# Kernel optimization log

Hardware: AMD Instinct MI355X
Metric: run time of the kernel (lower is better)

Reference implementation:

```python
import jax, jax.numpy as jnp
import numpy as np

N = 4096; IN = 78; OUT = 11
HN = 256; HB = 128; HM = 64; HV = 256; HU = 128
NOTES_PER_BEAT = 8; BEATS_PER_MEASURE = 4
NB = N // NOTES_PER_BEAT; NM = NB // BEATS_PER_MEASURE
UIN = 2*HN + 2*HB + 2*HM + 2*HV + OUT + 2 + 1 + 2   # output-LSTM input = 1424
BT_IN = 2*HB + 1 + 1 + 2 + 3 + (OUT - 1)            # tempo-LSTM input = 273
QPM_PRIMO_IDX = 5; TEMPO_IDX = 28


def _u(key, shape, k):
    return jax.random.uniform(key, shape, minval=-k, maxval=k, dtype=jnp.float32)


def _lstm_p(key, din, h, bidir):
    k = 1.0 / np.sqrt(h); n = 2 if bidir else 1
    k1, k2, k3 = jax.random.split(key, 3)
    Wi = _u(k1, (n, 4*h, din), k); Wh = _u(k2, (n, 4*h, h), k); b = _u(k3, (n, 4*h), k)
    if not bidir:
        Wi, Wh, b = Wi[0], Wh[0], b[0]
    return Wi, Wh, b


def _lin_p(key, din, dout):
    k = 1.0 / np.sqrt(din)
    k1, k2 = jax.random.split(key)
    return _u(k1, (dout, din), k), _u(k2, (dout,), k)


def setup_inputs():
    ks = jax.random.split(jax.random.key(0), 20)
    inp = {}
    inp['x'] = jax.random.normal(ks[0], (1, N, IN), dtype=jnp.float32)
    inp['y'] = jax.random.normal(ks[1], (1, 1, OUT), dtype=jnp.float32)
    inp['beat_ids'] = (jnp.arange(N) // NOTES_PER_BEAT).astype(jnp.int32)
    inp['measure_ids'] = (jnp.arange(N) // (NOTES_PER_BEAT * BEATS_PER_MEASURE)).astype(jnp.int32)
    inp['note_Wi'], inp['note_Wh'], inp['note_b'] = _lstm_p(ks[2], IN, HN, True)
    inp['voice_Wi'], inp['voice_Wh'], inp['voice_b'] = _lstm_p(ks[3], IN, HV, True)
    inp['beat_Wi'], inp['beat_Wh'], inp['beat_b'] = _lstm_p(ks[4], 2*HN, HB, True)
    inp['meas_Wi'], inp['meas_Wh'], inp['meas_b'] = _lstm_p(ks[5], 2*HB, HM, True)
    inp['Wba'], inp['bba'] = _lin_p(ks[6], 2*HN, 2*HN)
    inp['Wma'], inp['bma'] = _lin_p(ks[7], 2*HB, 2*HB)
    inp['Wta'], inp['bta'] = _lin_p(ks[8], OUT-1, OUT-1)
    inp['out_Wi'], inp['out_Wh'], inp['out_b'] = _lstm_p(ks[9], UIN, HU, False)
    inp['Wfc'], inp['bfc'] = _lin_p(ks[10], HU + UIN, OUT-1)
    inp['bt_Wi'], inp['bt_Wh'], inp['bt_b'] = _lstm_p(ks[11], BT_IN, HB, False)
    inp['Wt1'], inp['bt1'] = _lin_p(ks[12], HB, HB)
    inp['Wt2'], inp['bt2'] = _lin_p(ks[13], HB, 1)
    return inp


def _cell(h, c, xt, Wi, Wh, b):
    g = Wi @ xt + Wh @ h + b
    i, f, gg, o = jnp.split(g, 4)
    c2 = jax.nn.sigmoid(f) * c + jax.nn.sigmoid(i) * jnp.tanh(gg)
    return jax.nn.sigmoid(o) * jnp.tanh(c2), c2


def _lstm(xs, Wi, Wh, b, reverse=False):
    H = Wh.shape[-1]
    def step(carry, xt):
        h, c = _cell(carry[0], carry[1], xt, Wi, Wh, b)
        return (h, c), h
    init = (jnp.zeros(H, xs.dtype), jnp.zeros(H, xs.dtype))
    _, hs = jax.lax.scan(step, init, xs, reverse=reverse)
    return hs


def _bilstm(xs, Wi, Wh, b):
    return jnp.concatenate([_lstm(xs, Wi[0], Wh[0], b[0]),
                            _lstm(xs, Wi[1], Wh[1], b[1], reverse=True)], axis=-1)


def _seg_attn(h, seg, nseg, W, b):
    # sum_with_attention: softmax over group members, per feature dim (torch softmax dim=0)
    logits = h @ W.T + b
    m = jax.ops.segment_max(logits, seg, num_segments=nseg)
    e = jnp.exp(logits - m[seg])
    s = jax.ops.segment_sum(e, seg, num_segments=nseg)
    return jax.ops.segment_sum(h * (e / s[seg]), seg, num_segments=nseg)


def _forward(x, y, beat_ids, measure_ids, note_Wi, note_Wh, note_b, voice_Wi, voice_Wh, voice_b,
             beat_Wi, beat_Wh, beat_b, meas_Wi, meas_Wh, meas_b, Wba, bba, Wma, bma, Wta, bta,
             out_Wi, out_Wh, out_b, Wfc, bfc, bt_Wi, bt_Wh, bt_b, Wt1, bt1, Wt2, bt2):
    xs = x[0]                                   # [N, IN]
    note_h = _bilstm(xs, note_Wi, note_Wh, note_b)          # [N, 2*HN]
    voice_h = _bilstm(xs, voice_Wi, voice_Wh, voice_b)      # single voice -> whole seq
    beat_nodes = _seg_attn(note_h, beat_ids, NB, Wba, bba)  # [NB, 2*HN]
    beat_h = _bilstm(beat_nodes, beat_Wi, beat_Wh, beat_b)  # [NB, 2*HB]
    meas_of_beat = jax.ops.segment_min(measure_ids, beat_ids, num_segments=NB)
    meas_nodes = _seg_attn(beat_h, meas_of_beat, NM, Wma, bma)
    meas_h = _bilstm(meas_nodes, meas_Wi, meas_Wh, meas_b)  # [NM, 2*HM]

    qpm_primo = x[:, 0, QPM_PRIMO_IDX]          # (1,)
    tempo_primo = x[0, 0, -2:]                  # (2,)
    btv = xs[:, TEMPO_IDX:TEMPO_IDX+3]          # [N, 3]
    beat_pn = beat_h[beat_ids]                  # [N, 2*HB]
    meas_pn = meas_h[measure_ids]               # [N, 2*HM]
    is_b = jnp.concatenate([jnp.array([True]), beat_ids[1:] > beat_ids[:-1]])
    y_tail = y[0, 0, 1:]

    def step(carry, inp):
        buf, count, pt, th, tc, oh, oc, po, pv = carry
        nh_i, bh_i, mh_i, vh_i, btv_i, isb = inp
        # --- beat boundary: tempo attention + tempo LSTM step ---
        mask = jnp.arange(NOTES_PER_BEAT) < count
        logits = jnp.where(mask[:, None], buf @ Wta.T + bta, -1e9)
        att = jax.nn.softmax(logits, axis=0)
        result_node = jnp.where(count > 0, jnp.sum(buf * att, axis=0), y_tail)
        cat = jnp.concatenate([bh_i, pt, qpm_primo, tempo_primo, btv_i, result_node])
        nth, ntc = _cell(th, tc, cat, bt_Wi, bt_Wh, bt_b)
        tmp = Wt2 @ jax.nn.relu(Wt1 @ nth + bt1) + bt2     # (1,)
        th = jnp.where(isb, nth, th); tc = jnp.where(isb, ntc, tc)
        pt = jnp.where(isb, tmp, pt)
        buf = jnp.where(isb, jnp.zeros_like(buf), buf)
        count = jnp.where(isb, 0, count)
        comb = jnp.concatenate([nh_i, bh_i, mh_i, vh_i, po, pv, qpm_primo, tempo_primo])  # (UIN,)
        noh, noc = _cell(oh, oc, comb, out_Wi, out_Wh, out_b)
        out_fc = Wfc @ jnp.concatenate([noh, comb]) + bfc   # (OUT-1,)
        out = jnp.concatenate([pt, out_fc])                 # (OUT,)
        buf = buf.at[count].set(out_fc)
        return (buf, count + 1, pt, th, tc, noh, noc, out, out_fc[:2]), out

    carry0 = (jnp.zeros((NOTES_PER_BEAT, OUT-1)), jnp.array(0, jnp.int32), y[:, 0, 0],
              jnp.zeros(HB), jnp.zeros(HB), jnp.zeros(HU), jnp.zeros(HU), y[0, 0, :], jnp.zeros(2))
    _, outs = jax.lax.scan(step, carry0, (note_h, beat_pn, meas_pn, voice_h, btv, is_b))
    return outs[None], note_h[None]


def reference(x, y, beat_ids, measure_ids, note_Wi, note_Wh, note_b, voice_Wi, voice_Wh, voice_b,
              beat_Wi, beat_Wh, beat_b, meas_Wi, meas_Wh, meas_b, Wba, bba, Wma, bma, Wta, bta,
              out_Wi, out_Wh, out_b, Wfc, bfc, bt_Wi, bt_Wh, bt_b, Wt1, bt1, Wt2, bt2):
    return _forward(x, y, beat_ids, measure_ids, note_Wi, note_Wh, note_b, voice_Wi, voice_Wh, voice_b,
                    beat_Wi, beat_Wh, beat_b, meas_Wi, meas_Wh, meas_b, Wba, bba, Wma, bma, Wta, bta,
                    out_Wi, out_Wh, out_b, Wfc, bfc, bt_Wi, bt_Wh, bt_b, Wt1, bt1, Wt2, bt2)
```

## Files before the change

kernel.cpp:

```cpp
#include <hip/hip_runtime.h>
#include <hip/hip_bf16.h>

typedef unsigned int u32;
typedef _Float16 h16;
typedef __attribute__((ext_vector_type(2))) _Float16 h16x2;

union U4 { uint4 u; h16x2 p[4]; };

static __device__ __forceinline__ float sigm(float x){ return 1.0f / (1.0f + __expf(-x)); }
static __device__ __forceinline__ float ftanh(float x){ return 1.0f - 2.0f/(1.0f + __expf(2.0f*x)); }
static __device__ __forceinline__ h16x2 f2h2(float a, float b){
  h16x2 r; r[0] = (h16)a; r[1] = (h16)b; return r;
}
static __device__ __forceinline__ void pinv(h16x2 &x){
  u32 t = __builtin_bit_cast(u32, x);
  asm volatile("" : "+v"(t));
  x = __builtin_bit_cast(h16x2, t);
}

#if defined(__has_builtin)
#if __has_builtin(__builtin_amdgcn_fdot2)
#define FDOT2_NATIVE 1
#endif
#endif
static __device__ __forceinline__ float fdot2(h16x2 a, h16x2 b, float c){
#ifdef FDOT2_NATIVE
  return __builtin_amdgcn_fdot2(a, b, c, false);
#else
  return c + (float)a[0]*(float)b[0] + (float)a[1]*(float)b[1];
#endif
}

#define NT 4096
#define OUTS_OFF 45056

__global__ __launch_bounds__(256) void k0_prep(
    const float* __restrict__ noteWh, const float* __restrict__ voiceWh,
    const float* __restrict__ outWi,  const float* __restrict__ Wfc,
    h16* __restrict__ WhF, h16* __restrict__ outWiF, h16* __restrict__ WfcKF)
{
  const int NWH = 4*1024*256;
  const int NOW = 512*1416;
  const int NFC = 10*1416;
  for (int i = blockIdx.x*256 + threadIdx.x; i < NWH + NOW + NFC; i += gridDim.x*256) {
    if (i < NWH) {
      int dir = i >> 18;
      int rem = i & 262143;
      const float* src = (dir < 2) ? noteWh : voiceWh;
      WhF[i] = (h16)src[((dir & 1) << 18) + rem];
    } else if (i < NWH + NOW) {
      int j = i - NWH;
      int r = j / 1416, c = j - r*1416;
      float v = 0.f;
      if (c < 1408) v = outWi[(size_t)r*1424 + c];
      else if (c < 1411) v = outWi[(size_t)r*1424 + 1421 + (c-1408)];
      outWiF[j] = (h16)v;
    } else {
      int j = i - NWH - NOW;
      int r = j / 1416, c = j - r*1416;
      float v = 0.f;
      if (c < 1408) v = Wfc[(size_t)r*1552 + 128 + c];
      else if (c < 1411) v = Wfc[(size_t)r*1552 + 1549 + (c-1408)];
      WfcKF[j] = (h16)v;
    }
  }
}

__global__ __launch_bounds__(256) void k1_xgates(
    const float* __restrict__ x,
    const float* __restrict__ noteWi, const float* __restrict__ noteB,
    const float* __restrict__ voiceWi, const float* __restrict__ voiceB,
    h16* __restrict__ preNV)
{
  const int dir = blockIdx.y;
  const int t0  = blockIdx.x * 16;
  const int tid = threadIdx.x;
  __shared__ float xs[16][80];
  for (int i = tid; i < 16*78; i += 256) {
    int tt = i / 78, j = i - tt*78;
    xs[tt][j] = x[(size_t)(t0+tt)*78 + j];
  }
  __syncthreads();
  const float* Wi = (dir < 2) ? noteWi : voiceWi;
  const float* B  = (dir < 2) ? noteB  : voiceB;
  const int dw = dir & 1;
  for (int gc = 0; gc < 4; ++gc) {
    int g = gc*256 + tid;
    const float* row = Wi + ((size_t)dw*1024 + g)*78;
    float bias = B[dw*1024 + g];
    float acc[16];
#pragma unroll
    for (int tt=0; tt<16; ++tt) acc[tt] = bias;
#pragma unroll 6
    for (int j=0; j<78; ++j) {
      float w = row[j];
#pragma unroll
      for (int tt=0; tt<16; ++tt)
        acc[tt] += w*xs[tt][j];
    }
#pragma unroll
    for (int tt=0; tt<16; ++tt)
      preNV[((size_t)dir*NT + (t0+tt))*1024 + g] = (h16)acc[tt];
  }
}

__global__ __launch_bounds__(512) void k2_nvrec(
    const h16* __restrict__ WhF,
    const h16* __restrict__ preNV,
    float* __restrict__ note_h,
    float* __restrict__ voice_h,
    float* __restrict__ out_noteh)
{
  const int dir = blockIdx.x;
  const int L = threadIdx.x;
  const int r0 = L, r1 = L + 512;
  const h16* Wb = WhF + (size_t)dir*1024*256;

  h16x2 w0[88], w1[88];
#pragma unroll
  for (int c=0;c<22;++c){
    U4 a; a.u = *(const uint4*)(Wb + (size_t)r0*256 + c*8);
    U4 b; b.u = *(const uint4*)(Wb + (size_t)r1*256 + c*8);
#pragma unroll
    for (int i=0;i<4;++i){ w0[c*4+i]=a.p[i]; w1[c*4+i]=b.p[i]; }
  }
#pragma unroll
  for (int c=0;c<88;++c){ pinv(w0[c]); pinv(w1[c]); }
  __shared__ __align__(16) h16 Whl[1024*24];
  __shared__ __align__(16) h16 hb[256];
  __shared__ float gl[1024];
  for (int i = L; i < 1024*24; i += 512) {
    int r = i / 24, c = i - r*24;
    Whl[i] = Wb[(size_t)r*256 + 176 + c];
  }
  if (L < 256) hb[L] = (h16)0.f;
  float cc = 0.f;
  __syncthreads();

  const bool fwd = ((dir & 1) == 0);
  const bool isNote = (dir < 2);
  float* hout = isNote ? note_h : voice_h;
  const int half = (dir & 1) * 256;
  const h16* pre = preNV + (size_t)dir*NT*1024;
  const h16* sbase0 = Wb + (size_t)r0*256 + 200;
  const h16* sbase1 = Wb + (size_t)r1*256 + 200;

  for (int it = 0; it < NT; ++it) {
    const int t = fwd ? it : (NT-1) - it;
    U4 sa[7];
#pragma unroll
    for (int k=0;k<7;++k) sa[k].u = *(const uint4*)(sbase0 + k*8);
    float p0 = (float)pre[(size_t)t*1024 + r0];
    float p1 = (float)pre[(size_t)t*1024 + r1];
    float a0c[4] = {0.f,0.f,0.f,0.f};
    float a1c[4] = {0.f,0.f,0.f,0.f};
#pragma unroll
    for (int c=0;c<22;++c){
      U4 hh; hh.u = *(const uint4*)&hb[c*8];
#pragma unroll
      for (int i=0;i<4;++i){
        a0c[i] = fdot2(w0[c*4+i], hh.p[i], a0c[i]);
        a1c[i] = fdot2(w1[c*4+i], hh.p[i], a1c[i]);
      }
    }
#pragma unroll
    for (int c=0;c<3;++c){
      U4 la; la.u = *(const uint4*)&Whl[r0*24 + c*8];
      U4 lb; lb.u = *(const uint4*)&Whl[r1*24 + c*8];
      U4 hh; hh.u = *(const uint4*)&hb[176 + c*8];
#pragma unroll
      for (int i=0;i<4;++i){
        a0c[i] = fdot2(la.p[i], hh.p[i], a0c[i]);
        a1c[i] = fdot2(lb.p[i], hh.p[i], a1c[i]);
      }
    }
#pragma unroll
    for (int k=0;k<7;++k){
      U4 hh; hh.u = *(const uint4*)&hb[200 + k*8];
#pragma unroll
      for (int i=0;i<4;++i) a0c[i] = fdot2(sa[k].p[i], hh.p[i], a0c[i]);
    }
    U4 sb[7];
#pragma unroll
    for (int k=0;k<7;++k) sb[k].u = *(const uint4*)(sbase1 + k*8);
#pragma unroll
    for (int k=0;k<7;++k){
      U4 hh; hh.u = *(const uint4*)&hb[200 + k*8];
#pragma unroll
      for (int i=0;i<4;++i) a1c[i] = fdot2(sb[k].p[i], hh.p[i], a1c[i]);
    }
    gl[r0] = p0 + ((a0c[0]+a0c[1]) + (a0c[2]+a0c[3]));
    gl[r1] = p1 + ((a1c[0]+a1c[1]) + (a1c[2]+a1c[3]));
    __syncthreads();
    if (L < 256) {
      float gi = gl[L], gf = gl[L+256], gg = gl[L+512], go = gl[L+768];
      cc = sigm(gf)*cc + sigm(gi)*ftanh(gg);
      float h = sigm(go)*ftanh(cc);
      hb[L] = (h16)h;
      hout[(size_t)t*512 + half + L] = h;
      if (isNote) out_noteh[(size_t)t*512 + half + L] = h;
    }
    __syncthreads();
  }
}

__global__ __launch_bounds__(256) void k3_battn(
    const float* __restrict__ note_h,
    const float* __restrict__ Wba, const float* __restrict__ bba,
    float* __restrict__ beat_nodes)
{
  const int b = blockIdx.x;
  const int tid = threadIdx.x;
  __shared__ float nh[8][512];
  for (int i = tid; i < 8*512; i += 256)
    nh[i>>9][i&511] = note_h[(size_t)b*8*512 + i];
  __syncthreads();
  for (int dc = 0; dc < 2; ++dc) {
    int d = dc*256 + tid;
    const float* wr = Wba + (size_t)d*512;
    float bb = bba[d];
    float l[8];
#pragma unroll
    for (int n=0;n<8;++n) l[n]=bb;
#pragma unroll 4
    for (int j=0; j<512; ++j) {
      float w = wr[j];
#pragma unroll
      for (int n=0;n<8;++n) l[n] += w*nh[n][j];
    }
    float m = l[0];
#pragma unroll
    for (int n=1;n<8;++n) m = fmaxf(m, l[n]);
    float s = 0.f, o = 0.f;
#pragma unroll
    for (int n=0;n<8;++n) { float e = __expf(l[n]-m); s += e; o += e*nh[n][d]; }
    beat_nodes[(size_t)b*512 + d] = o / s;
  }
}

__global__ __launch_bounds__(256) void k4_bgates(
    const float* __restrict__ beat_nodes,
    const float* __restrict__ beatWi, const float* __restrict__ beatB,
    float* __restrict__ preB)
{
  const int dir = blockIdx.y, b0 = blockIdx.x*8, tid = threadIdx.x;
  __shared__ float nd[8][512];
  for (int i = tid; i < 8*512; i += 256)
    nd[i>>9][i&511] = beat_nodes[(size_t)b0*512 + i];
  __syncthreads();
  for (int gc = 0; gc < 2; ++gc) {
    int g = gc*256 + tid;
    const float* wr = beatWi + ((size_t)dir*512 + g)*512;
    float bias = beatB[dir*512 + g];
    float acc[8];
#pragma unroll
    for (int n=0;n<8;++n) acc[n]=bias;
#pragma unroll 4
    for (int j=0; j<512; ++j) {
      float w = wr[j];
#pragma unroll
      for (int n=0;n<8;++n) acc[n] += w*nd[n][j];
    }
#pragma unroll
    for (int n=0;n<8;++n)
      preB[((size_t)dir*512 + (b0+n))*512 + g] = acc[n];
  }
}

__global__ __launch_bounds__(512) void k5_brec(
    const float* __restrict__ beatWh,
    const float* __restrict__ preB,
    float* __restrict__ beat_h)
{
  const int dir = blockIdx.x, L = threadIdx.x;
  h16x2 w[64];
  {
    const float2* p = (const float2*)(beatWh + ((size_t)dir*512 + L)*128);
#pragma unroll
    for (int c=0;c<64;++c){
      float2 v = p[c];
      w[c] = f2h2(v.x, v.y);
    }
  }
#pragma unroll
  for (int c=0;c<64;++c) pinv(w[c]);
  __shared__ __align__(16) h16 hb[128];
  __shared__ float gl[512];
  if (L < 128) hb[L] = (h16)0.f;
  float cc = 0.f;
  __syncthreads();
  const bool fwd = (dir == 0);
  for (int it = 0; it < 512; ++it) {
    const int t = fwd ? it : 511 - it;
    float pr = preB[((size_t)dir*512 + t)*512 + L];
    float ac[4] = {0.f,0.f,0.f,0.f};
#pragma unroll
    for (int c=0;c<16;++c){
      U4 hh; hh.u = *(const uint4*)&hb[c*8];
#pragma unroll
      for (int i=0;i<4;++i) ac[i] = fdot2(w[c*4+i], hh.p[i], ac[i]);
    }
    gl[L] = pr + ((ac[0]+ac[1]) + (ac[2]+ac[3]));
    __syncthreads();
    if (L < 128) {
      float gi = gl[L], gf = gl[L+128], gg = gl[L+256], go = gl[L+384];
      cc = sigm(gf)*cc + sigm(gi)*ftanh(gg);
      float h = sigm(go)*ftanh(cc);
      hb[L] = (h16)h;
      beat_h[(size_t)t*256 + dir*128 + L] = h;
    }
    __syncthreads();
  }
}

__global__ __launch_bounds__(256) void k6_mattn(
    const float* __restrict__ beat_h,
    const float* __restrict__ Wma, const float* __restrict__ bma,
    float* __restrict__ meas_nodes)
{
  const int m = blockIdx.x, tid = threadIdx.x;
  __shared__ float bh[4][256];
  for (int i = tid; i < 4*256; i += 256)
    bh[i>>8][i&255] = beat_h[(size_t)m*4*256 + i];
  __syncthreads();
  int d = tid;
  const float* wr = Wma + (size_t)d*256;
  float bb = bma[d];
  float l[4];
#pragma unroll
  for (int n=0;n<4;++n) l[n]=bb;
#pragma unroll 4
  for (int j=0; j<256; ++j) {
    float w = wr[j];
#pragma unroll
    for (int n=0;n<4;++n) l[n] += w*bh[n][j];
  }
  float mm = fmaxf(fmaxf(l[0],l[1]), fmaxf(l[2],l[3]));
  float s = 0.f, o = 0.f;
#pragma unroll
  for (int n=0;n<4;++n) { float e = __expf(l[n]-mm); s += e; o += e*bh[n][d]; }
  meas_nodes[(size_t)m*256 + d] = o / s;
}

__global__ __launch_bounds__(256) void k7_mgates(
    const float* __restrict__ meas_nodes,
    const float* __restrict__ measWi, const float* __restrict__ measB,
    float* __restrict__ preM)
{
  const int dir = blockIdx.y, m0 = blockIdx.x*8, tid = threadIdx.x;
  __shared__ float nd[8][256];
  for (int i = tid; i < 8*256; i += 256)
    nd[i>>8][i&255] = meas_nodes[(size_t)m0*256 + i];
  __syncthreads();
  int g = tid;
  const float* wr = measWi + ((size_t)dir*256 + g)*256;
  float bias = measB[dir*256 + g];
  float acc[8];
#pragma unroll
  for (int n=0;n<8;++n) acc[n]=bias;
#pragma unroll 4
  for (int j=0; j<256; ++j) {
    float w = wr[j];
#pragma unroll
    for (int n=0;n<8;++n) acc[n] += w*nd[n][j];
  }
#pragma unroll
  for (int n=0;n<8;++n)
    preM[((size_t)dir*128 + (m0+n))*256 + g] = acc[n];
}

__global__ __launch_bounds__(256, 2) void k8_mrec(
    const float* __restrict__ measWh,
    const float* __restrict__ preM,
    float* __restrict__ meas_h)
{
  const int dir = blockIdx.x, L = threadIdx.x;
  h16x2 w[32];
  {
    const float2* p = (const float2*)(measWh + ((size_t)dir*256 + L)*64);
#pragma unroll
    for (int c=0;c<32;++c){
      float2 v = p[c];
      w[c] = f2h2(v.x, v.y);
    }
  }
#pragma unroll
  for (int c=0;c<32;++c) pinv(w[c]);
  __shared__ __align__(16) h16 hb[64];
  __shared__ float gl[256];
  if (L < 64) hb[L] = (h16)0.f;
  float cc = 0.f;
  __syncthreads();
  const bool fwd = (dir == 0);
  for (int it = 0; it < 128; ++it) {
    const int t = fwd ? it : 127 - it;
    float pr = preM[((size_t)dir*128 + t)*256 + L];
    float ac[4] = {0.f,0.f,0.f,0.f};
#pragma unroll
    for (int c=0;c<8;++c){
      U4 hh; hh.u = *(const uint4*)&hb[c*8];
#pragma unroll
      for (int i=0;i<4;++i) ac[i] = fdot2(w[c*4+i], hh.p[i], ac[i]);
    }
    gl[L] = pr + ((ac[0]+ac[1]) + (ac[2]+ac[3]));
    __syncthreads();
    if (L < 64) {
      float gi = gl[L], gf = gl[L+64], gg = gl[L+128], go = gl[L+192];
      cc = sigm(gf)*cc + sigm(gi)*ftanh(gg);
      float h = sigm(go)*ftanh(cc);
      hb[L] = (h16)h;
      meas_h[(size_t)t*128 + dir*64 + L] = h;
    }
    __syncthreads();
  }
}

__global__ __launch_bounds__(256) void k9_scanpre(
    const float* __restrict__ note_h, const float* __restrict__ voice_h,
    const float* __restrict__ beat_h, const float* __restrict__ meas_h,
    const float* __restrict__ xf,
    const h16* __restrict__ outWiF, const h16* __restrict__ WfcKF,
    const float* __restrict__ outB, const float* __restrict__ bfc,
    float* __restrict__ pre_out, float* __restrict__ pre_fc)
{
  const int t0 = blockIdx.x*8, tid = threadIdx.x;
  __shared__ __align__(16) h16 kn[8][1416];
  const float qpm = xf[5], tp0 = xf[76], tp1 = xf[77];
  for (int i = tid; i < 8*1416; i += 256) {
    int tt = i/1416, c = i - tt*1416;
    int t = t0 + tt;
    float v;
    if (c < 512) v = note_h[(size_t)t*512 + c];
    else if (c < 768) v = beat_h[(size_t)(t>>3)*256 + (c-512)];
    else if (c < 896) v = meas_h[(size_t)(t>>5)*128 + (c-768)];
    else if (c < 1408) v = voice_h[(size_t)t*512 + (c-896)];
    else if (c == 1408) v = qpm;
    else if (c == 1409) v = tp0;
    else if (c == 1410) v = tp1;
    else v = 0.f;
    kn[tt][c] = (h16)v;
  }
  __syncthreads();
  for (int rr = 0; rr < 3; ++rr) {
    int r = (rr < 2) ? (tid + rr*256) : (512 + tid);
    if (rr == 2 && tid >= 10) break;
    const h16* wrow = (r < 512) ? (outWiF + (size_t)r*1416) : (WfcKF + (size_t)(r-512)*1416);
    float bias = (r < 512) ? outB[r] : bfc[r-512];
    float acc[8];
#pragma unroll
    for (int tt=0;tt<8;++tt) acc[tt] = bias;
    for (int cu = 0; cu < 177; ++cu) {
      U4 wv; wv.u = *(const uint4*)(wrow + cu*8);
#pragma unroll
      for (int tt=0; tt<8; ++tt) {
        U4 kv; kv.u = *(const uint4*)&kn[tt][cu*8];
#pragma unroll
        for (int i=0;i<4;++i) acc[tt] = fdot2(wv.p[i], kv.p[i], acc[tt]);
      }
    }
#pragma unroll
    for (int tt=0; tt<8; ++tt) {
      if (r < 512) pre_out[(size_t)(t0+tt)*512 + r] = acc[tt];
      else pre_fc[(size_t)(t0+tt)*16 + (r-512)] = acc[tt];
    }
  }
}

__global__ __launch_bounds__(256) void k9b_btpre(
    const float* __restrict__ beat_h, const float* __restrict__ xf,
    const float* __restrict__ btWi, const float* __restrict__ btB,
    float* __restrict__ pre_bt)
{
  const int b0 = blockIdx.x*8, tid = threadIdx.x;
  __shared__ float bh[8][256];
  __shared__ float btv[8][3];
  for (int i = tid; i < 8*256; i += 256)
    bh[i>>8][i&255] = beat_h[(size_t)b0*256 + i];
  if (tid < 24) {
    int n = tid/3, j = tid - n*3;
    btv[n][j] = xf[(size_t)(b0+n)*8*78 + 28 + j];
  }
  __syncthreads();
  const float qpm = xf[5], tp0 = xf[76], tp1 = xf[77];
  for (int gc = 0; gc < 2; ++gc) {
    int g = gc*256 + tid;
    const float* row = btWi + (size_t)g*273;
    float bias = btB[g];
    float acc[8];
#pragma unroll
    for (int n=0;n<8;++n) acc[n]=bias;
#pragma unroll 4
    for (int j = 0; j < 256; ++j) {
      float w = row[j];
#pragma unroll
      for (int n=0;n<8;++n) acc[n] += w*bh[n][j];
    }
    float w257 = row[257], w258 = row[258], w259 = row[259];
    float w260 = row[260], w261 = row[261], w262 = row[262];
#pragma unroll
    for (int n=0;n<8;++n) {
      acc[n] += w257*qpm + w258*tp0 + w259*tp1
              + w260*btv[n][0] + w261*btv[n][1] + w262*btv[n][2];
      pre_bt[(size_t)(b0+n)*512 + g] = acc[n];
    }
  }
}

__global__ __launch_bounds__(512) void k10_scan(
    const float* __restrict__ pre_out, const float* __restrict__ pre_fc,
    const float* __restrict__ pre_bt,
    const float* __restrict__ outWh, const float* __restrict__ btWh,
    const float* __restrict__ outWi, const float* __restrict__ btWi,
    const float* __restrict__ Wfc,
    const float* __restrict__ Wta, const float* __restrict__ bta,
    const float* __restrict__ Wt1, const float* __restrict__ bt1,
    const float* __restrict__ Wt2, const float* __restrict__ bt2,
    const float* __restrict__ yf,
    float* __restrict__ out)
{
  const int L = threadIdx.x;
  h16x2 owh[64], btw[64];
  {
    const float2* p = (const float2*)(outWh + (size_t)L*128);
    const float2* q = (const float2*)(btWh + (size_t)L*128);
#pragma unroll
    for (int c=0;c<64;++c){
      float2 a = p[c]; owh[c] = f2h2(a.x, a.y);
      float2 b = q[c]; btw[c] = f2h2(b.x, b.y);
    }
  }
#pragma unroll
  for (int c=0;c<64;++c){ pinv(owh[c]); pinv(btw[c]); }
  float oseq[13];
#pragma unroll
  for (int j=0;j<13;++j) oseq[j] = outWi[(size_t)L*1424 + 1408 + j];
  float btpt = btWi[(size_t)L*273 + 256];
  float btrn[10];
#pragma unroll
  for (int d=0;d<10;++d) btrn[d] = btWi[(size_t)L*273 + 263 + d];

  __shared__ __align__(16) h16 oh16[128];
  __shared__ __align__(16) h16 th16[128];
  __shared__ __align__(16) h16 Wt1f[128*136];
  __shared__ __align__(16) h16 WfcD[10*128];
  __shared__ float gl[512], gb[512];
  __shared__ float pofc[16];
  __shared__ float ptvS;
  __shared__ float buf[8][10];
  __shared__ float rn[10], att[8][10], r1v[128], ytail[10];
  __shared__ float WfcSeq[10][13];
  __shared__ float WtaS[100], btaS[10], Wt2S[128], bt1S[128], bt2S;

  for (int i=L; i<128*128; i+=512) Wt1f[(i>>7)*136 + (i&127)] = (h16)Wt1[i];
  for (int i=L; i<10*128; i+=512)  WfcD[i] = (h16)Wfc[(size_t)(i>>7)*1552 + (i&127)];
  if (L < 100) WtaS[L] = Wta[L];
  if (L < 10)  btaS[L] = bta[L];
  if (L < 128) { Wt2S[L] = Wt2[L]; bt1S[L] = bt1[L]; }
  if (L == 0)  bt2S = bt2[0];
  if (L < 128) { oh16[L] = (h16)0.f; th16[L] = (h16)0.f; }
  if (L < 11) pofc[L] = yf[L];
  if (L >= 11 && L < 16) pofc[L] = 0.f;
  if (L == 0) ptvS = yf[0];
  if (L < 10) ytail[L] = yf[1+L];
  if (L < 80) buf[L/10][L%10] = 0.f;
  if (L < 130) WfcSeq[L/13][L%13] = Wfc[(size_t)(L/13)*1552 + 1536 + (L%13)];
  float oc = 0.f, tc = 0.f;
  const int dD = L >> 2, qD = L & 3;
  float prv  = pre_out[L];
  float prbt = pre_bt[L];
  float prfc = (L < 40 && qD == 0) ? pre_fc[dD] : 0.f;
  __syncthreads();

  for (int t = 0; t < NT; ++t) {
    const bool isb = (t & 7) == 0;
    if (isb) {
      if (t == 0) {
        if (L < 10) rn[L] = ytail[L];
      } else {
        if (L < 80) {
          int n = L/10, d = L - n*10;
          float s = btaS[d];
#pragma unroll
          for (int j=0;j<10;++j) s += buf[n][j]*WtaS[d*10 + j];
          att[n][d] = s;
        }
        __syncthreads();
        if (L < 10) {
          float m = att[0][L];
#pragma unroll
          for (int n=1;n<8;++n) m = fmaxf(m, att[n][L]);
          float s = 0.f, acc = 0.f;
#pragma unroll
          for (int n=0;n<8;++n) { float e = __expf(att[n][L]-m); s += e; acc += e*buf[n][L]; }
          rn[L] = acc/s;
        }
      }
      __syncthreads();
    }
    {
      float pr = prv;
      if (t+1 < NT) prv = pre_out[(size_t)(t+1)*512 + L];
      float ac[4] = {0.f,0.f,0.f,0.f};
#pragma unroll
      for (int c=0;c<16;++c){
        U4 hh; hh.u = *(const uint4*)&oh16[c*8];
#pragma unroll
        for (int i=0;i<4;++i) ac[i] = fdot2(owh[c*4+i], hh.p[i], ac[i]);
      }
      float a = pr + ((ac[0]+ac[1]) + (ac[2]+ac[3]));
#pragma unroll
      for (int j=0;j<13;++j) a += oseq[j]*pofc[j];
      gl[L] = a;
    }
    if (isb) {
      float pr = prbt + btpt*ptvS;
      if (t+8 < NT) prbt = pre_bt[(size_t)((t>>3)+1)*512 + L];
      float ac[4] = {0.f,0.f,0.f,0.f};
#pragma unroll
      for (int c=0;c<16;++c){
        U4 hh; hh.u = *(const uint4*)&th16[c*8];
#pragma unroll
        for (int i=0;i<4;++i) ac[i] = fdot2(btw[c*4+i], hh.p[i], ac[i]);
      }
      float b = pr + ((ac[0]+ac[1]) + (ac[2]+ac[3]));
#pragma unroll
      for (int d=0;d<10;++d) b += btrn[d]*rn[d];
      gb[L] = b;
    }
    __syncthreads();
    if (L < 128) {
      float gi = gl[L], gf = gl[L+128], gg = gl[L+256], go = gl[L+384];
      oc = sigm(gf)*oc + sigm(gi)*ftanh(gg);
      float nh = sigm(go)*ftanh(oc);
      oh16[L] = (h16)nh;
    } else if (L < 256 && isb) {
      int j = L - 128;
      float gi = gb[j], gf = gb[j+128], gg = gb[j+256], go = gb[j+384];
      tc = sigm(gf)*tc + sigm(gi)*ftanh(gg);
      float nth = sigm(go)*ftanh(tc);
      th16[j] = (h16)nth;
    }
    __syncthreads();
    if (isb) {
      if (L < 128) {
        float ac[4] = {0.f,0.f,0.f,0.f};
        const h16* wrow = &Wt1f[L*136];
#pragma unroll
        for (int k=0;k<16;++k){
          U4 wv; wv.u = *(const uint4*)(wrow + k*8);
          U4 hh; hh.u = *(const uint4*)&th16[k*8];
#pragma unroll
          for (int i=0;i<4;++i) ac[i] = fdot2(wv.p[i], hh.p[i], ac[i]);
        }
        float s = bt1S[L] + ((ac[0]+ac[1]) + (ac[2]+ac[3]));
        r1v[L] = fmaxf(s, 0.f);
      }
      __syncthreads();
    }
    if (L < 64) {
      float ptv_l;
      if (isb) {
        float p = Wt2S[L]*r1v[L] + Wt2S[L+64]*r1v[L+64];
#pragma unroll
        for (int sft=32; sft>0; sft>>=1) p += __shfl_xor(p, sft, 64);
        ptv_l = p + bt2S;
        if (L == 0) ptvS = ptv_l;
      } else {
        ptv_l = ptvS;
      }
      float s = 0.f;
      if (L < 40) {
        const h16* wr = &WfcD[dD*128 + qD*32];
#pragma unroll
        for (int j=0;j<32;++j) s += (float)wr[j] * (float)oh16[qD*32 + j];
      }
      s += __shfl_xor(s, 1, 64);
      s += __shfl_xor(s, 2, 64);
      float e = 0.f;
      if (L < 40 && qD == 0) {
        e = prfc;
#pragma unroll
        for (int j=0;j<13;++j) e += WfcSeq[dD][j]*pofc[j];
        if (t+1 < NT) prfc = pre_fc[(size_t)(t+1)*16 + dD];
      }
      float ofc = s + e;
      int srcE = (L >= 1 && L < 11) ? 4*(L-1) : ((L >= 11 && L < 13) ? 4*(L-11) : 0);
      float valE = __shfl(ofc, srcE, 64);
      float bval = __shfl(ofc, 4*(L & 15), 64);
      if (L == 0)      { out[(size_t)t*11] = ptv_l; pofc[0] = ptv_l; }
      else if (L < 11) { out[(size_t)t*11 + L] = valE; pofc[L] = valE; }
      else if (L < 13) { pofc[L] = valE; }
      if (L < 10) buf[t & 7][L] = bval;
    }
    __syncthreads();
  }
}

extern "C" void kernel_launch(void* const* d_in, const int* in_sizes, int n_in,
                              void* d_out, int out_size, void* d_ws, size_t ws_size,
                              hipStream_t stream)
{
  const float* x      = (const float*)d_in[0];
  const float* y      = (const float*)d_in[1];
  const float* noteWi = (const float*)d_in[4];
  const float* noteWh = (const float*)d_in[5];
  const float* noteB  = (const float*)d_in[6];
  const float* voiceWi= (const float*)d_in[7];
  const float* voiceWh= (const float*)d_in[8];
  const float* voiceB = (const float*)d_in[9];
  const float* beatWi = (const float*)d_in[10];
  const float* beatWh = (const float*)d_in[11];
  const float* beatB  = (const float*)d_in[12];
  const float* measWi = (const float*)d_in[13];
  const float* measWh = (const float*)d_in[14];
  const float* measB  = (const float*)d_in[15];
  const float* Wba    = (const float*)d_in[16];
  const float* bba    = (const float*)d_in[17];
  const float* Wma    = (const float*)d_in[18];
  const float* bma    = (const float*)d_in[19];
  const float* Wta    = (const float*)d_in[20];
  const float* bta    = (const float*)d_in[21];
  const float* outWi  = (const float*)d_in[22];
  const float* outWh  = (const float*)d_in[23];
  const float* outB   = (const float*)d_in[24];
  const float* Wfc    = (const float*)d_in[25];
  const float* bfc    = (const float*)d_in[26];
  const float* btWi   = (const float*)d_in[27];
  const float* btWh   = (const float*)d_in[28];
  const float* btB    = (const float*)d_in[29];
  const float* Wt1    = (const float*)d_in[30];
  const float* bt1    = (const float*)d_in[31];
  const float* Wt2    = (const float*)d_in[32];
  const float* bt2    = (const float*)d_in[33];

  float* fws = (float*)d_ws;
  float* note_h     = fws + 0;
  float* voice_h    = fws + 2097152;
  float* beat_nodes = fws + 4194304;
  float* preB       = fws + 4456448;
  float* beat_h     = fws + 4980736;
  float* meas_nodes = fws + 5111808;
  float* preM       = fws + 5144576;
  float* meas_h     = fws + 5210112;
  float* pre_out    = fws + 5226496;
  float* pre_fc     = fws + 7323648;
  float* pre_bt     = fws + 7389184;
  h16* hws   = (h16*)(fws + 7651328);
  h16* preNV  = hws;
  h16* WhF    = hws + 16777216;
  h16* outWiF = hws + 17825792;
  h16* WfcKF  = hws + 18550784;

  float* out_outs  = (float*)d_out;
  float* out_noteh = out_outs + OUTS_OFF;

  hipLaunchKernelGGL(k0_prep, dim3(1024), dim3(256), 0, stream,
                     noteWh, voiceWh, outWi, Wfc, WhF, outWiF, WfcKF);
  hipLaunchKernelGGL(k1_xgates, dim3(256,4), dim3(256), 0, stream,
                     x, noteWi, noteB, voiceWi, voiceB, preNV);
  hipLaunchKernelGGL(k2_nvrec, dim3(4), dim3(512), 0, stream,
                     WhF, preNV, note_h, voice_h, out_noteh);
  hipLaunchKernelGGL(k3_battn, dim3(512), dim3(256), 0, stream,
                     note_h, Wba, bba, beat_nodes);
  hipLaunchKernelGGL(k4_bgates, dim3(64,2), dim3(256), 0, stream,
                     beat_nodes, beatWi, beatB, preB);
  hipLaunchKernelGGL(k5_brec, dim3(2), dim3(512), 0, stream,
                     beatWh, preB, beat_h);
  hipLaunchKernelGGL(k6_mattn, dim3(128), dim3(256), 0, stream,
                     beat_h, Wma, bma, meas_nodes);
  hipLaunchKernelGGL(k7_mgates, dim3(16,2), dim3(256), 0, stream,
                     meas_nodes, measWi, measB, preM);
  hipLaunchKernelGGL(k8_mrec, dim3(2), dim3(256), 0, stream,
                     measWh, preM, meas_h);
  hipLaunchKernelGGL(k9b_btpre, dim3(64), dim3(256), 0, stream,
                     beat_h, x, btWi, btB, pre_bt);
  hipLaunchKernelGGL(k9_scanpre, dim3(512), dim3(256), 0, stream,
                     note_h, voice_h, beat_h, meas_h, x, outWiF, WfcKF, outB, bfc, pre_out, pre_fc);
  hipLaunchKernelGGL(k10_scan, dim3(1), dim3(512), 0, stream,
                     pre_out, pre_fc, pre_bt, outWh, btWh, outWi, btWi, Wfc,
                     Wta, bta, Wt1, bt1, Wt2, bt2, y, out_outs);
}
```

Measured before the change: 16.34 ms.

## Restructure note/voice LSTM recurrence so each thread computes all four gates

Changes the work split in the recurrent kernel: each thread pair owns one hidden unit and holds half of all four gate rows in registers, split by column half, with the rest of the weights in LDS. Partial sums are combined with a cross-lane shuffle instead of a shared gate buffer. The hidden state is double-buffered, so each timestep needs one barrier instead of two. The precompute kernel now writes gate-interleaved pre-activations so each thread fetches its four gates in one load, prefetched one step ahead. This trades the per-step global weight streaming and the extra sync for higher register pressure.

```diff
diff --git a/kernel.cpp b/kernel.cpp
--- a/kernel.cpp
+++ b/kernel.cpp
@@ -100,11 +100,11 @@
     }
 #pragma unroll
     for (int tt=0; tt<16; ++tt)
-      preNV[((size_t)dir*NT + (t0+tt))*1024 + g] = (h16)acc[tt];
-  }
-}
-
-__global__ __launch_bounds__(512) void k2_nvrec(
+      preNV[((size_t)dir*NT + (t0+tt))*1024 + (tid*4 + gc)] = (h16)acc[tt];
+  }
+}
+
+__global__ __launch_bounds__(512, 2) void k2_nvrec(
     const h16* __restrict__ WhF,
     const h16* __restrict__ preNV,
     float* __restrict__ note_h,
@@ -113,27 +113,39 @@
 {
   const int dir = blockIdx.x;
   const int L = threadIdx.x;
-  const int r0 = L, r1 = L + 512;
+  const int lane = L & 63;
+  const int wid  = L >> 6;
+  const int hi   = lane >> 5;
+  const int e    = wid*32 + (lane & 31);
+  const int c0   = hi*128;
   const h16* Wb = WhF + (size_t)dir*1024*256;
 
-  h16x2 w0[88], w1[88];
-#pragma unroll
-  for (int c=0;c<22;++c){
-    U4 a; a.u = *(const uint4*)(Wb + (size_t)r0*256 + c*8);
-    U4 b; b.u = *(const uint4*)(Wb + (size_t)r1*256 + c*8);
-#pragma unroll
-    for (int i=0;i<4;++i){ w0[c*4+i]=a.p[i]; w1[c*4+i]=b.p[i]; }
-  }
-#pragma unroll
-  for (int c=0;c<88;++c){ pinv(w0[c]); pinv(w1[c]); }
-  __shared__ __align__(16) h16 Whl[1024*24];
-  __shared__ __align__(16) h16 hb[256];
-  __shared__ float gl[1024];
-  for (int i = L; i < 1024*24; i += 512) {
-    int r = i / 24, c = i - r*24;
-    Whl[i] = Wb[(size_t)r*256 + 176 + c];
-  }
-  if (L < 256) hb[L] = (h16)0.f;
+  h16x2 w[4][48];
+#pragma unroll
+  for (int g=0; g<4; ++g) {
+    const h16* row = Wb + (size_t)(g*256 + e)*256 + c0;
+#pragma unroll
+    for (int cb=0; cb<12; ++cb) {
+      U4 a; a.u = *(const uint4*)(row + cb*8);
+#pragma unroll
+      for (int i=0;i<4;++i) w[g][cb*4+i] = a.p[i];
+    }
+  }
+#pragma unroll
+  for (int g=0; g<4; ++g)
+#pragma unroll
+    for (int c=0;c<48;++c) pinv(w[g][c]);
+
+  __shared__ __align__(16) h16 Wl[4*4*2*256*8];
+  __shared__ __align__(16) h16 hb[2][256];
+#pragma unroll
+  for (int cb=0; cb<4; ++cb)
+#pragma unroll
+    for (int g=0; g<4; ++g) {
+      const h16* src = Wb + (size_t)(g*256 + e)*256 + c0 + 96 + cb*8;
+      *(uint4*)&Wl[(size_t)((((cb*4+g)*2 + hi)*256 + e))*8] = *(const uint4*)src;
+    }
+  if (hi == 0) hb[0][e] = (h16)0.f;
   float cc = 0.f;
   __syncthreads();
 
@@ -142,64 +154,58 @@
   float* hout = isNote ? note_h : voice_h;
   const int half = (dir & 1) * 256;
   const h16* pre = preNV + (size_t)dir*NT*1024;
-  const h16* sbase0 = Wb + (size_t)r0*256 + 200;
-  const h16* sbase1 = Wb + (size_t)r1*256 + 200;
-
-  for (int it = 0; it < NT; ++it) {
-    const int t = fwd ? it : (NT-1) - it;
-    U4 sa[7];
-#pragma unroll
-    for (int k=0;k<7;++k) sa[k].u = *(const uint4*)(sbase0 + k*8);
-    float p0 = (float)pre[(size_t)t*1024 + r0];
-    float p1 = (float)pre[(size_t)t*1024 + r1];
-    float a0c[4] = {0.f,0.f,0.f,0.f};
-    float a1c[4] = {0.f,0.f,0.f,0.f};
-#pragma unroll
-    for (int c=0;c<22;++c){
-      U4 hh; hh.u = *(const uint4*)&hb[c*8];
-#pragma unroll
-      for (int i=0;i<4;++i){
-        a0c[i] = fdot2(w0[c*4+i], hh.p[i], a0c[i]);
-        a1c[i] = fdot2(w1[c*4+i], hh.p[i], a1c[i]);
-      }
-    }
-#pragma unroll
-    for (int c=0;c<3;++c){
-      U4 la; la.u = *(const uint4*)&Whl[r0*24 + c*8];
-      U4 lb; lb.u = *(const uint4*)&Whl[r1*24 + c*8];
-      U4 hh; hh.u = *(const uint4*)&hb[176 + c*8];
-#pragma unroll
-      for (int i=0;i<4;++i){
-        a0c[i] = fdot2(la.p[i], hh.p[i], a0c[i]);
-        a1c[i] = fdot2(lb.p[i], hh.p[i], a1c[i]);
-      }
-    }
-#pragma unroll
-    for (int k=0;k<7;++k){
-      U4 hh; hh.u = *(const uint4*)&hb[200 + k*8];
-#pragma unroll
-      for (int i=0;i<4;++i) a0c[i] = fdot2(sa[k].p[i], hh.p[i], a0c[i]);
-    }
-    U4 sb[7];
-#pragma unroll
-    for (int k=0;k<7;++k) sb[k].u = *(const uint4*)(sbase1 + k*8);
-#pragma unroll
-    for (int k=0;k<7;++k){
-      U4 hh; hh.u = *(const uint4*)&hb[200 + k*8];
-#pragma unroll
-      for (int i=0;i<4;++i) a1c[i] = fdot2(sb[k].p[i], hh.p[i], a1c[i]);
-    }
-    gl[r0] = p0 + ((a0c[0]+a0c[1]) + (a0c[2]+a0c[3]));
-    gl[r1] = p1 + ((a1c[0]+a1c[1]) + (a1c[2]+a1c[3]));
-    __syncthreads();
-    if (L < 256) {
-      float gi = gl[L], gf = gl[L+256], gg = gl[L+512], go = gl[L+768];
-      cc = sigm(gf)*cc + sigm(gi)*ftanh(gg);
-      float h = sigm(go)*ftanh(cc);
-      hb[L] = (h16)h;
-      hout[(size_t)t*512 + half + L] = h;
-      if (isNote) out_noteh[(size_t)t*512 + half + L] = h;
-    }
+  int cur = 0;
+  const int step = fwd ? 1 : -1;
+  int t = fwd ? 0 : NT-1;
+
+  union PU { uint2 u; h16 h[4]; };
+  PU pv_n; pv_n.u = *(const uint2*)(pre + (size_t)t*1024 + e*4);
+
+  for (int it = 0; it < NT; ++it, t += step) {
+    PU pv = pv_n;
+    if (it+1 < NT) pv_n.u = *(const uint2*)(pre + (size_t)(t+step)*1024 + e*4);
+
+    float ac[4][2] = {{0.f,0.f},{0.f,0.f},{0.f,0.f},{0.f,0.f}};
+#pragma unroll
+    for (int cb=0; cb<12; ++cb) {
+      U4 hh; hh.u = *(const uint4*)&hb[cur][c0 + cb*8];
+#pragma unroll
+      for (int i=0;i<4;++i) {
+        ac[0][i&1] = fdot2(w[0][cb*4+i], hh.p[i], ac[0][i&1]);
+        ac[1][i&1] = fdot2(w[1][cb*4+i], hh.p[i], ac[1][i&1]);
+        ac[2][i&1] = fdot2(w[2][cb*4+i], hh.p[i], ac[2][i&1]);
+        ac[3][i&1] = fdot2(w[3][cb*4+i], hh.p[i], ac[3][i&1]);
+      }
+    }
+#pragma unroll
+    for (int cb=0; cb<4; ++cb) {
+      U4 hh; hh.u = *(const uint4*)&hb[cur][c0 + 96 + cb*8];
+#pragma unroll
+      for (int g=0; g<4; ++g) {
+        U4 wv; wv.u = *(const uint4*)&Wl[(size_t)((((cb*4+g)*2 + hi)*256 + e))*8];
+#pragma unroll
+        for (int i=0;i<4;++i) ac[g][i&1] = fdot2(wv.p[i], hh.p[i], ac[g][i&1]);
+      }
+    }
+    float g4[4];
+#pragma unroll
+    for (int g=0; g<4; ++g) {
+      float s = ac[g][0] + ac[g][1];
+      s += __shfl_xor(s, 32, 64);
+      g4[g] = s;
+    }
+    float gi = (float)pv.h[0] + g4[0];
+    float gf = (float)pv.h[1] + g4[1];
+    float gg = (float)pv.h[2] + g4[2];
+    float go = (float)pv.h[3] + g4[3];
+    cc = sigm(gf)*cc + sigm(gi)*ftanh(gg);
+    float h = sigm(go)*ftanh(cc);
+    if (hi == 0) {
+      hb[cur^1][e] = (h16)h;
+      hout[(size_t)t*512 + half + e] = h;
+      if (isNote) out_noteh[(size_t)t*512 + half + e] = h;
+    }
+    cur ^= 1;
     __syncthreads();
   }
 }
```

After: 14.80 ms. 1.1x faster.
